# Optimization experiments

Hardware: AMD Instinct MI355X
Metric: run time of the kernel (lower is better)

Reference implementation:

```python
import jax, jax.numpy as jnp
import numpy as np

SEQ, BATCH, IN, HID = 512, 64, 1024, 1024

def setup_inputs() -> dict:
    key = jax.random.key(0)
    k0, k1, k2, k3, k4 = jax.random.split(key, 5)
    k = 1.0 / np.sqrt(HID).astype(np.float32)
    x = jax.random.normal(k0, (SEQ, BATCH, IN), dtype=jnp.float32)
    W_ih = jax.random.uniform(k1, (HID, IN), jnp.float32, -k, k)
    W_hh = jax.random.uniform(k2, (HID, HID), jnp.float32, -k, k)
    b_ih = jax.random.uniform(k3, (HID,), jnp.float32, -k, k)
    b_hh = jax.random.uniform(k4, (HID,), jnp.float32, -k, k)
    return {"x": x, "W_ih": W_ih, "W_hh": W_hh, "b_ih": b_ih, "b_hh": b_hh}

def reference(x, W_ih, W_hh, b_ih, b_hh):
    # Elman RNN: h_t = tanh(x_t @ W_ih^T + h_{t-1} @ W_hh^T + b_ih + b_hh)
    B = x.shape[1]
    H = W_hh.shape[0]
    # Precompute all input projections in one big GEMM: [S,B,H]
    xW = jnp.einsum('sbi,hi->sbh', x, W_ih) + (b_ih + b_hh)
    W_hh_T = W_hh.T
    def step(h, xw_t):
        h_new = jnp.tanh(xw_t + h @ W_hh_T)
        return h_new, h_new
    h0 = jnp.zeros((B, H), dtype=x.dtype)
    h_last, out = jax.lax.scan(step, h0, xW)
    # output: [S,B,H]; h_n: [1,B,H]
    return out, h_last[None, :, :]
```

## Files before the change

kernel.cpp:

```cpp
#include <hip/hip_runtime.h>

typedef short short8 __attribute__((ext_vector_type(8)));
typedef float f32x4 __attribute__((ext_vector_type(4)));
typedef unsigned short us4 __attribute__((ext_vector_type(4)));

#define SQ 512
#define BA 64
#define HD 1024
#define NWG 64
#define NCTR 8
#define CTR_STRIDE 64

__device__ __forceinline__ unsigned short f2bf(float f) {
    unsigned u = __float_as_uint(f);
    u += 0x7fffu + ((u >> 16) & 1u);
    return (unsigned short)(u >> 16);
}
__device__ __forceinline__ float bf2f(unsigned short h) {
    return __uint_as_float(((unsigned)h) << 16);
}
__device__ __forceinline__ void waitcnt_vm0() {
    asm volatile("s_waitcnt vmcnt(0)" ::: "memory");
}
__device__ __forceinline__ short8 ld_frag(const unsigned short* p) {
    const unsigned long long* q = (const unsigned long long*)p;
    unsigned long long a = __hip_atomic_load(q,     __ATOMIC_RELAXED, __HIP_MEMORY_SCOPE_AGENT);
    unsigned long long b = __hip_atomic_load(q + 1, __ATOMIC_RELAXED, __HIP_MEMORY_SCOPE_AGENT);
    union { unsigned long long u[2]; short8 v; } cv;
    cv.u[0] = a; cv.u[1] = b;
    return cv.v;
}

__global__ void __launch_bounds__(256) xw_gemm(
    const float* __restrict__ x, const float* __restrict__ Wih,
    const float* __restrict__ bih, const float* __restrict__ bhh,
    float* __restrict__ out, unsigned* __restrict__ ctr)
{
    if (blockIdx.x == 0 && blockIdx.y == 0 && threadIdx.x < NCTR)
        ctr[threadIdx.x * CTR_STRIDE] = 0u;

    __shared__ unsigned short Ahi[128][40];
    __shared__ unsigned short Alo[128][40];
    __shared__ unsigned short Bhi[128][40];
    __shared__ unsigned short Blo[128][40];

    const int tid  = threadIdx.x;
    const int lane = tid & 63, wid = tid >> 6;
    const int bx = blockIdx.x, by = blockIdx.y;
    const int wm = (wid & 1) * 64, wn = (wid >> 1) * 64;
    const int rf = lane & 15, bq = lane >> 4, kf = bq * 8;

    f32x4 acc[4][4] = {};

    const int srow = tid >> 3;
    const int scol = (tid & 7) * 4;
    const float* aBase = x   + (size_t)(bx * 128 + srow) * HD + scol;
    const float* bBase = Wih + (size_t)(by * 128 + srow) * HD + scol;

    for (int kc = 0; kc < 32; ++kc) {
        __syncthreads();
        const int ko = kc * 32;
#pragma unroll
        for (int i = 0; i < 4; ++i) {
            const int r = srow + i * 32;
            float4 av = *(const float4*)(aBase + (size_t)(i * 32) * HD + ko);
            float4 bv = *(const float4*)(bBase + (size_t)(i * 32) * HD + ko);
            us4 ah, al, bh, bl;
            ah.x = f2bf(av.x); al.x = f2bf(av.x - bf2f(ah.x));
            ah.y = f2bf(av.y); al.y = f2bf(av.y - bf2f(ah.y));
            ah.z = f2bf(av.z); al.z = f2bf(av.z - bf2f(ah.z));
            ah.w = f2bf(av.w); al.w = f2bf(av.w - bf2f(ah.w));
            bh.x = f2bf(bv.x); bl.x = f2bf(bv.x - bf2f(bh.x));
            bh.y = f2bf(bv.y); bl.y = f2bf(bv.y - bf2f(bh.y));
            bh.z = f2bf(bv.z); bl.z = f2bf(bv.z - bf2f(bh.z));
            bh.w = f2bf(bv.w); bl.w = f2bf(bv.w - bf2f(bh.w));
            *(us4*)&Ahi[r][scol] = ah;
            *(us4*)&Alo[r][scol] = al;
            *(us4*)&Bhi[r][scol] = bh;
            *(us4*)&Blo[r][scol] = bl;
        }
        __syncthreads();

        short8 afh[4], afl[4], bfh[4], bfl[4];
#pragma unroll
        for (int i = 0; i < 4; ++i) {
            afh[i] = *(const short8*)&Ahi[wm + 16 * i + rf][kf];
            afl[i] = *(const short8*)&Alo[wm + 16 * i + rf][kf];
            bfh[i] = *(const short8*)&Bhi[wn + 16 * i + rf][kf];
            bfl[i] = *(const short8*)&Blo[wn + 16 * i + rf][kf];
        }
#pragma unroll
        for (int i = 0; i < 4; ++i)
#pragma unroll
            for (int j = 0; j < 4; ++j) {
                acc[i][j] = __builtin_amdgcn_mfma_f32_16x16x32_bf16(afh[i], bfh[j], acc[i][j], 0, 0, 0);
                acc[i][j] = __builtin_amdgcn_mfma_f32_16x16x32_bf16(afh[i], bfl[j], acc[i][j], 0, 0, 0);
                acc[i][j] = __builtin_amdgcn_mfma_f32_16x16x32_bf16(afl[i], bfh[j], acc[i][j], 0, 0, 0);
            }
    }

#pragma unroll
    for (int j = 0; j < 4; ++j) {
        const int col = by * 128 + wn + 16 * j + rf;
        const float bias = bih[col] + bhh[col];
#pragma unroll
        for (int i = 0; i < 4; ++i) {
            const int row0 = bx * 128 + wm + 16 * i + bq * 4;
#pragma unroll
            for (int r = 0; r < 4; ++r)
                out[(size_t)(row0 + r) * HD + col] = acc[i][j][r] + bias;
        }
    }
}

__global__ void __launch_bounds__(256) rnn_recurrence(
    const float* __restrict__ Whh,
    float* __restrict__ io,
    float* __restrict__ hn,
    unsigned short* __restrict__ hbuf,
    unsigned* __restrict__ ctr)
{
    __shared__ unsigned short Whi[16][1032];
    __shared__ unsigned short Wlo[16][1032];

    const int tid = threadIdx.x;
    const int h0  = blockIdx.x * 16;

    for (int i = tid; i < 16 * 1024; i += 256) {
        const int r = i >> 10, c = i & 1023;
        const float w = Whh[(size_t)(h0 + r) * HD + c];
        const unsigned short hi = f2bf(w);
        Whi[r][c] = hi;
        Wlo[r][c] = f2bf(w - bf2f(hi));
    }
    __syncthreads();

    const int lane = tid & 63, wid = tid >> 6;
    const int rf = lane & 15, bq = lane >> 4, kf = bq * 8;

    unsigned short* H0 = hbuf;
    unsigned short* H1 = hbuf + BA * HD;

    const int bslot = (blockIdx.x & (NCTR - 1)) * CTR_STRIDE;
    const int brow  = wid * 16 + bq * 4;
    const int col   = h0 + rf;

    float v[4];
    unsigned hi4[4];

#pragma unroll
    for (int r = 0; r < 4; ++r) {
        v[r] = tanhf(io[(size_t)(brow + r) * HD + col]);
        hi4[r] = f2bf(v[r]);
    }
#pragma unroll
    for (int r = 0; r < 4; ++r) {
        const unsigned oh = __shfl_xor(hi4[r], 1);
        if ((lane & 1) == 0) {
            const size_t e = ((size_t)(brow + r) * HD + col) >> 1;
            __hip_atomic_store((unsigned*)H0 + e, (hi4[r] & 0xffffu) | (oh << 16),
                               __ATOMIC_RELAXED, __HIP_MEMORY_SCOPE_AGENT);
        }
    }

    float xwv[4];
#pragma unroll
    for (int r = 0; r < 4; ++r)
        xwv[r] = io[(size_t)(BA * HD) + (size_t)(brow + r) * HD + col];

    const int ab = wid * 16 + rf;

    for (int t = 1; t < SQ; ++t) {
        waitcnt_vm0();
        __syncthreads();
        if (tid == 0)
            __hip_atomic_fetch_add(ctr + bslot, 1u, __ATOMIC_RELAXED, __HIP_MEMORY_SCOPE_AGENT);

        float* outP = io + (size_t)(t - 1) * (BA * HD);
#pragma unroll
        for (int r = 0; r < 4; ++r)
            outP[(size_t)(brow + r) * HD + col] = v[r];

        float xwn[4] = {0.f, 0.f, 0.f, 0.f};
        if (t + 1 < SQ) {
            const float* nxt = io + (size_t)(t + 1) * (BA * HD);
#pragma unroll
            for (int r = 0; r < 4; ++r)
                xwn[r] = nxt[(size_t)(brow + r) * HD + col];
        }

        if (tid == 0) {
            const unsigned target = (unsigned)(NWG) * (unsigned)t;
            unsigned s;
            do {
                s = 0;
#pragma unroll
                for (int c = 0; c < NCTR; ++c)
                    s += __hip_atomic_load(ctr + c * CTR_STRIDE,
                                           __ATOMIC_RELAXED, __HIP_MEMORY_SCOPE_AGENT);
            } while (s < target);
        }
        __syncthreads();

        const unsigned short* Ph = (t & 1) ? H0 : H1;
        unsigned short*       Nh = (t & 1) ? H1 : H0;

        const unsigned short* ap = Ph + (size_t)ab * HD + kf;

        f32x4 acc = {};
#pragma unroll 8
        for (int kc = 0; kc < 32; ++kc) {
            short8 Af = ld_frag(ap + kc * 32);
            short8 Bh = *(const short8*)&Whi[rf][kc * 32 + kf];
            short8 Bl = *(const short8*)&Wlo[rf][kc * 32 + kf];
            acc = __builtin_amdgcn_mfma_f32_16x16x32_bf16(Af, Bh, acc, 0, 0, 0);
            acc = __builtin_amdgcn_mfma_f32_16x16x32_bf16(Af, Bl, acc, 0, 0, 0);
        }

#pragma unroll
        for (int r = 0; r < 4; ++r) {
            v[r] = tanhf(acc[r] + xwv[r]);
            hi4[r] = f2bf(v[r]);
            xwv[r] = xwn[r];
        }
#pragma unroll
        for (int r = 0; r < 4; ++r) {
            const unsigned oh = __shfl_xor(hi4[r], 1);
            if ((lane & 1) == 0) {
                const size_t e = ((size_t)(brow + r) * HD + col) >> 1;
                __hip_atomic_store((unsigned*)Nh + e, (hi4[r] & 0xffffu) | (oh << 16),
                                   __ATOMIC_RELAXED, __HIP_MEMORY_SCOPE_AGENT);
            }
        }
    }

    float* outL = io + (size_t)(SQ - 1) * (BA * HD);
#pragma unroll
    for (int r = 0; r < 4; ++r) {
        const size_t o = (size_t)(brow + r) * HD + col;
        outL[o] = v[r];
        hn[o]   = v[r];
    }
}

extern "C" void kernel_launch(void* const* d_in, const int* in_sizes, int n_in,
                              void* d_out, int out_size, void* d_ws, size_t ws_size,
                              hipStream_t stream) {
    const float* x   = (const float*)d_in[0];
    const float* Wih = (const float*)d_in[1];
    const float* Whh = (const float*)d_in[2];
    const float* bih = (const float*)d_in[3];
    const float* bhh = (const float*)d_in[4];

    float* io = (float*)d_out;
    float* hn = io + (size_t)SQ * BA * HD;

    unsigned* ctr = (unsigned*)d_ws;
    unsigned short* hbuf = (unsigned short*)((char*)d_ws + 4096);

    hipLaunchKernelGGL(xw_gemm, dim3(256, 8), dim3(256), 0, stream,
                       x, Wih, bih, bhh, io, ctr);

    void* args[] = {(void*)&Whh, (void*)&io, (void*)&hn, (void*)&hbuf, (void*)&ctr};
    hipLaunchCooperativeKernel((void*)rnn_recurrence, dim3(NWG), dim3(256),
                               args, 0, stream);
}
```

Before: 5.209 ms.

## Replace global step barrier with per-wave flags and fine-grained dependency waits

Drops the per-step atomic counter barrier and its two __syncthreads. Each wave now publishes a release flag once its slice of h_t is stored. Consumers poll only the 8 producer flags covering each 128-wide K chunk and load that chunk as soon as it is ready, so loads of early chunks overlap with waiting on later ones. The MFMA chain is also split into four independent accumulators to shorten the dependency chain. The gain relies on the point-to-point flags being correct under the relaxed/release memory ordering, and there is more polling traffic in exchange.

```diff
diff --git a/kernel.cpp b/kernel.cpp
--- a/kernel.cpp
+++ b/kernel.cpp
@@ -8,8 +8,7 @@
 #define BA 64
 #define HD 1024
 #define NWG 64
-#define NCTR 8
-#define CTR_STRIDE 64
+#define FSTR 16
 
 __device__ __forceinline__ unsigned short f2bf(float f) {
     unsigned u = __float_as_uint(f);
@@ -34,10 +33,10 @@
 __global__ void __launch_bounds__(256) xw_gemm(
     const float* __restrict__ x, const float* __restrict__ Wih,
     const float* __restrict__ bih, const float* __restrict__ bhh,
-    float* __restrict__ out, unsigned* __restrict__ ctr)
+    float* __restrict__ out, unsigned* __restrict__ flags)
 {
-    if (blockIdx.x == 0 && blockIdx.y == 0 && threadIdx.x < NCTR)
-        ctr[threadIdx.x * CTR_STRIDE] = 0u;
+    if (blockIdx.x == 0 && blockIdx.y == 0)
+        flags[threadIdx.x * FSTR] = 0u;
 
     __shared__ unsigned short Ahi[128][40];
     __shared__ unsigned short Alo[128][40];
@@ -113,18 +112,19 @@
     }
 }
 
-__global__ void __launch_bounds__(256) rnn_recurrence(
+__global__ void __launch_bounds__(256, 1) rnn_recurrence(
     const float* __restrict__ Whh,
     float* __restrict__ io,
     float* __restrict__ hn,
     unsigned short* __restrict__ hbuf,
-    unsigned* __restrict__ ctr)
+    unsigned* __restrict__ flags)
 {
     __shared__ unsigned short Whi[16][1032];
     __shared__ unsigned short Wlo[16][1032];
 
     const int tid = threadIdx.x;
-    const int h0  = blockIdx.x * 16;
+    const int bx  = blockIdx.x;
+    const int h0  = bx * 16;
 
     for (int i = tid; i < 16 * 1024; i += 256) {
         const int r = i >> 10, c = i & 1023;
@@ -141,12 +141,16 @@
     unsigned short* H0 = hbuf;
     unsigned short* H1 = hbuf + BA * HD;
 
-    const int bslot = (blockIdx.x & (NCTR - 1)) * CTR_STRIDE;
-    const int brow  = wid * 16 + bq * 4;
-    const int col   = h0 + rf;
+    const int brow = wid * 16 + bq * 4;
+    const int col  = h0 + rf;
+    const int ab   = wid * 16 + rf;
+
+    unsigned* myflag = flags + (size_t)(bx * 4 + wid) * FSTR;
+    const unsigned watchbase = (unsigned)((lane & 7) * 4 + wid) * FSTR;
 
     float v[4];
     unsigned hi4[4];
+    float xwv[4];
 
 #pragma unroll
     for (int r = 0; r < 4; ++r) {
@@ -162,20 +166,15 @@
                                __ATOMIC_RELAXED, __HIP_MEMORY_SCOPE_AGENT);
         }
     }
-
-    float xwv[4];
+    waitcnt_vm0();
+    if (lane == 0)
+        __hip_atomic_store(myflag, 1u, __ATOMIC_RELEASE, __HIP_MEMORY_SCOPE_AGENT);
+
 #pragma unroll
     for (int r = 0; r < 4; ++r)
         xwv[r] = io[(size_t)(BA * HD) + (size_t)(brow + r) * HD + col];
 
-    const int ab = wid * 16 + rf;
-
     for (int t = 1; t < SQ; ++t) {
-        waitcnt_vm0();
-        __syncthreads();
-        if (tid == 0)
-            __hip_atomic_fetch_add(ctr + bslot, 1u, __ATOMIC_RELAXED, __HIP_MEMORY_SCOPE_AGENT);
-
         float* outP = io + (size_t)(t - 1) * (BA * HD);
 #pragma unroll
         for (int r = 0; r < 4; ++r)
@@ -189,48 +188,61 @@
                 xwn[r] = nxt[(size_t)(brow + r) * HD + col];
         }
 
-        if (tid == 0) {
-            const unsigned target = (unsigned)(NWG) * (unsigned)t;
-            unsigned s;
-            do {
-                s = 0;
-#pragma unroll
-                for (int c = 0; c < NCTR; ++c)
-                    s += __hip_atomic_load(ctr + c * CTR_STRIDE,
-                                           __ATOMIC_RELAXED, __HIP_MEMORY_SCOPE_AGENT);
-            } while (s < target);
-        }
-        __syncthreads();
-
         const unsigned short* Ph = (t & 1) ? H0 : H1;
         unsigned short*       Nh = (t & 1) ? H1 : H0;
-
         const unsigned short* ap = Ph + (size_t)ab * HD + kf;
 
-        f32x4 acc = {};
-#pragma unroll 8
-        for (int kc = 0; kc < 32; ++kc) {
-            short8 Af = ld_frag(ap + kc * 32);
-            short8 Bh = *(const short8*)&Whi[rf][kc * 32 + kf];
-            short8 Bl = *(const short8*)&Wlo[rf][kc * 32 + kf];
-            acc = __builtin_amdgcn_mfma_f32_16x16x32_bf16(Af, Bh, acc, 0, 0, 0);
-            acc = __builtin_amdgcn_mfma_f32_16x16x32_bf16(Af, Bl, acc, 0, 0, 0);
+        short8 a[8][4];
+#pragma unroll
+        for (int g = 0; g < 8; ++g) {
+            const unsigned* fp = flags + watchbase + (unsigned)g * (32u * FSTR);
+            unsigned fv = __hip_atomic_load(fp, __ATOMIC_RELAXED, __HIP_MEMORY_SCOPE_AGENT);
+            while (!__all((int)(fv >= (unsigned)t)))
+                fv = __hip_atomic_load(fp, __ATOMIC_RELAXED, __HIP_MEMORY_SCOPE_AGENT);
+#pragma unroll
+            for (int i = 0; i < 4; ++i)
+                a[g][i] = ld_frag(ap + (size_t)(g * 4 + i) * 32);
+        }
+
+        f32x4 ah0 = {}, ah1 = {}, al0 = {}, al1 = {};
+#pragma unroll
+        for (int g = 0; g < 8; ++g) {
+#pragma unroll
+            for (int i = 0; i < 4; ++i) {
+                const int kc = g * 4 + i;
+                short8 bh = *(const short8*)&Whi[rf][kc * 32 + kf];
+                short8 bl = *(const short8*)&Wlo[rf][kc * 32 + kf];
+                if (i & 1) {
+                    ah1 = __builtin_amdgcn_mfma_f32_16x16x32_bf16(a[g][i], bh, ah1, 0, 0, 0);
+                    al1 = __builtin_amdgcn_mfma_f32_16x16x32_bf16(a[g][i], bl, al1, 0, 0, 0);
+                } else {
+                    ah0 = __builtin_amdgcn_mfma_f32_16x16x32_bf16(a[g][i], bh, ah0, 0, 0, 0);
+                    al0 = __builtin_amdgcn_mfma_f32_16x16x32_bf16(a[g][i], bl, al0, 0, 0, 0);
+                }
+            }
         }
 
 #pragma unroll
         for (int r = 0; r < 4; ++r) {
-            v[r] = tanhf(acc[r] + xwv[r]);
+            v[r] = tanhf(((ah0[r] + ah1[r]) + (al0[r] + al1[r])) + xwv[r]);
             hi4[r] = f2bf(v[r]);
             xwv[r] = xwn[r];
         }
-#pragma unroll
-        for (int r = 0; r < 4; ++r) {
-            const unsigned oh = __shfl_xor(hi4[r], 1);
-            if ((lane & 1) == 0) {
-                const size_t e = ((size_t)(brow + r) * HD + col) >> 1;
-                __hip_atomic_store((unsigned*)Nh + e, (hi4[r] & 0xffffu) | (oh << 16),
-                                   __ATOMIC_RELAXED, __HIP_MEMORY_SCOPE_AGENT);
+
+        if (t < SQ - 1) {
+#pragma unroll
+            for (int r = 0; r < 4; ++r) {
+                const unsigned oh = __shfl_xor(hi4[r], 1);
+                if ((lane & 1) == 0) {
+                    const size_t e = ((size_t)(brow + r) * HD + col) >> 1;
+                    __hip_atomic_store((unsigned*)Nh + e, (hi4[r] & 0xffffu) | (oh << 16),
+                                       __ATOMIC_RELAXED, __HIP_MEMORY_SCOPE_AGENT);
+                }
             }
+            waitcnt_vm0();
+            if (lane == 0)
+                __hip_atomic_store(myflag, (unsigned)(t + 1),
+                                   __ATOMIC_RELEASE, __HIP_MEMORY_SCOPE_AGENT);
         }
     }
 
@@ -255,13 +267,13 @@
     float* io = (float*)d_out;
     float* hn = io + (size_t)SQ * BA * HD;
 
-    unsigned* ctr = (unsigned*)d_ws;
-    unsigned short* hbuf = (unsigned short*)((char*)d_ws + 4096);
+    unsigned* flags = (unsigned*)d_ws;
+    unsigned short* hbuf = (unsigned short*)((char*)d_ws + 16384);
 
     hipLaunchKernelGGL(xw_gemm, dim3(256, 8), dim3(256), 0, stream,
-                       x, Wih, bih, bhh, io, ctr);
-
-    void* args[] = {(void*)&Whh, (void*)&io, (void*)&hn, (void*)&hbuf, (void*)&ctr};
+                       x, Wih, bih, bhh, io, flags);
+
+    void* args[] = {(void*)&Whh, (void*)&io, (void*)&hn, (void*)&hbuf, (void*)&flags};
     hipLaunchCooperativeKernel((void*)rnn_recurrence, dim3(NWG), dim3(256),
                                args, 0, stream);
 }
```

New measurement: 7.103 ms. 36.4% more time.
